# Kernel optimization log

Measured on AMD Instinct MI355X. Metric: run time of the kernel, lower is better.

Reference implementation:

```python
import jax, jax.numpy as jnp
import numpy as np

N_NODES = 100000
N_EDGES = 640000
D_IN = 128
D_HID = 128
D_OUT = 128
EPS = 1e-12  # F.normalize clamp_min eps


def _sage_conv(x, src, dst, Wl, bl, Wr):
    # mean aggregation of source features onto destination nodes
    msgs = x[src]                                              # [E, C] gather
    agg = jax.ops.segment_sum(msgs, dst, num_segments=N_NODES)  # [N, C] scatter-add
    cnt = jax.ops.segment_sum(jnp.ones((src.shape[0],), x.dtype), dst,
                              num_segments=N_NODES)
    agg = agg / jnp.maximum(cnt, 1.0)[:, None]
    out = agg @ Wl.T + bl + x @ Wr.T                           # lin_l(aggr) + lin_r(root)
    # L2 row-normalize (normalize=True)
    norm = jnp.sqrt(jnp.sum(out * out, axis=-1, keepdims=True))
    return out / jnp.maximum(norm, EPS)


def setup_inputs() -> dict:
    key = jax.random.key(0)
    ks = jax.random.split(key, 8)
    x = jax.random.normal(ks[0], (N_NODES, D_IN), dtype=jnp.float32)
    edge_index = jax.random.randint(ks[1], (2, N_EDGES), 0, N_NODES, dtype=jnp.int64)
    s1 = 1.0 / np.sqrt(D_IN)
    s2 = 1.0 / np.sqrt(D_HID)
    Wl1 = jax.random.uniform(ks[2], (D_HID, D_IN), jnp.float32, -s1, s1)
    bl1 = jax.random.uniform(ks[3], (D_HID,), jnp.float32, -s1, s1)
    Wr1 = jax.random.uniform(ks[4], (D_HID, D_IN), jnp.float32, -s1, s1)
    Wl2 = jax.random.uniform(ks[5], (D_OUT, D_HID), jnp.float32, -s2, s2)
    bl2 = jax.random.uniform(ks[6], (D_OUT,), jnp.float32, -s2, s2)
    Wr2 = jax.random.uniform(ks[7], (D_OUT, D_HID), jnp.float32, -s2, s2)
    return {"x": x, "edge_index": edge_index, "Wl1": Wl1, "bl1": bl1,
            "Wr1": Wr1, "Wl2": Wl2, "bl2": bl2, "Wr2": Wr2}


def reference(x, edge_index, Wl1, bl1, Wr1, Wl2, bl2, Wr2):
    src, dst = edge_index[0], edge_index[1]
    h = _sage_conv(x, src, dst, Wl1, bl1, Wr1)
    h = jax.nn.relu(h)  # dropout is identity in eval mode
    h = _sage_conv(h, src, dst, Wl2, bl2, Wr2)
    return h
```

## Files before the change

### kernel.cpp

```cpp
#include <hip/hip_runtime.h>
#include <hip/hip_bf16.h>
#include <stdint.h>

#define N_NODES 100000
#define N_EDGES 640000
#define MPAD    100096
#define CNT4_BLOCKS (N_EDGES / 1024)
#define CONV4_T     (N_NODES * 32)
#define CONV4_BLOCKS ((CONV4_T + 255) / 256)

typedef short  bf8_t  __attribute__((ext_vector_type(8)));
typedef float  f32x4  __attribute__((ext_vector_type(4)));

__device__ __forceinline__ unsigned f2bf(float f) {
  unsigned u = __builtin_bit_cast(unsigned, f);
  return ((u + 0x7fffu + ((u >> 16) & 1u)) >> 16) & 0xffffu;
}
__device__ __forceinline__ float bf2f(unsigned bits) {
  return __builtin_bit_cast(float, bits << 16);
}

__global__ void k_count_conv(const int* __restrict__ dst, int* __restrict__ cnt,
                             const float* __restrict__ x, unsigned* __restrict__ A1,
                             const float* __restrict__ Wl1, const float* __restrict__ Wr1,
                             unsigned short* __restrict__ Bf1,
                             const float* __restrict__ Wl2, const float* __restrict__ Wr2,
                             unsigned short* __restrict__ Bf2) {
  int bx = blockIdx.x;
  if (bx < CNT4_BLOCKS) {
    int base = bx * 1024 + threadIdx.x;
    int d0 = dst[base], d1 = dst[base + 256], d2 = dst[base + 512], d3 = dst[base + 768];
    atomicAdd(&cnt[d0], 1);
    atomicAdd(&cnt[d1], 1);
    atomicAdd(&cnt[d2], 1);
    atomicAdd(&cnt[d3], 1);
    return;
  }
  if (bx < CNT4_BLOCKS + CONV4_BLOCKS) {
    int i = (bx - CNT4_BLOCKS) * 256 + threadIdx.x;
    if (i < CONV4_T) {
      int w = i >> 5, t = i & 31;
      float4 f = ((const float4*)x)[i];
      uint2 u;
      u.x = f2bf(f.x) | (f2bf(f.y) << 16);
      u.y = f2bf(f.z) | (f2bf(f.w) << 16);
      ((uint2*)A1)[(size_t)w * 64 + 32 + t] = u;
    }
    return;
  }
  int gid = (bx - CNT4_BLOCKS - CONV4_BLOCKS) * 256 + threadIdx.x;
  if (gid >= 8192) return;
  int tid = gid & 4095;
  const float* Wl = (gid < 4096) ? Wl1 : Wl2;
  const float* Wr = (gid < 4096) ? Wr1 : Wr2;
  unsigned short* Bf = (gid < 4096) ? Bf1 : Bf2;
  int lane = tid & 63;
  int t  = (tid >> 6) & 7;
  int kc = tid >> 9;
  int c = lane & 15, q = lane >> 4;
  int col = t * 16 + c;
  for (int j = 0; j < 8; ++j) {
    int k = kc * 32 + q * 8 + j;
    float v = (k < 128) ? Wl[col * 128 + k] : Wr[col * 128 + (k - 128)];
    Bf[(size_t)tid * 8 + j] = (unsigned short)f2bf(v);
  }
}

__global__ void k_bsum(const int* __restrict__ cnt, int* __restrict__ bsum) {
  __shared__ int s[256];
  int base = blockIdx.x * 1024;
  int t = threadIdx.x;
  int v = 0;
  for (int j = 0; j < 4; ++j) {
    int i = base + j * 256 + t;
    if (i < N_NODES) v += cnt[i];
  }
  s[t] = v; __syncthreads();
  for (int o = 128; o > 0; o >>= 1) { if (t < o) s[t] += s[t + o]; __syncthreads(); }
  if (t == 0) bsum[blockIdx.x] = s[0];
}

__global__ void k_scanb(int* __restrict__ bsum, int nb) {
  __shared__ int s[128];
  int t = threadIdx.x;
  int v = (t < nb) ? bsum[t] : 0;
  s[t] = v; __syncthreads();
  for (int o = 1; o < 128; o <<= 1) {
    int add = (t >= o) ? s[t - o] : 0;
    __syncthreads();
    s[t] += add;
    __syncthreads();
  }
  if (t < nb) bsum[t] = s[t] - v;
}

__global__ void k_scanchunk(const int* __restrict__ cnt, const int* __restrict__ bsum,
                            int* __restrict__ rowptr, float* __restrict__ inv,
                            int* __restrict__ cursor) {
  __shared__ int s[1024];
  int t = threadIdx.x;
  int i = blockIdx.x * 1024 + t;
  int v = (i < N_NODES) ? cnt[i] : 0;
  s[t] = v; __syncthreads();
  for (int o = 1; o < 1024; o <<= 1) {
    int add = (t >= o) ? s[t - o] : 0;
    __syncthreads();
    s[t] += add;
    __syncthreads();
  }
  int incl = s[t];
  int bofs = bsum[blockIdx.x];
  if (i < N_NODES) {
    int start = bofs + incl - v;
    rowptr[i] = start;
    inv[i] = 1.0f / fmaxf((float)v, 1.0f);
    cursor[i] = start;
  }
  if (i == N_NODES - 1) rowptr[N_NODES] = bofs + incl;
}

__global__ void k_scatter(const int* __restrict__ src, const int* __restrict__ dst,
                          int* __restrict__ cursor, int* __restrict__ esrc) {
  int base = blockIdx.x * 1024 + threadIdx.x;
  int d0 = dst[base],       d1 = dst[base + 256];
  int d2 = dst[base + 512], d3 = dst[base + 768];
  int s0 = src[base],       s1 = src[base + 256];
  int s2 = src[base + 512], s3 = src[base + 768];
  int p0 = atomicAdd(&cursor[d0], 1);
  int p1 = atomicAdd(&cursor[d1], 1);
  int p2 = atomicAdd(&cursor[d2], 1);
  int p3 = atomicAdd(&cursor[d3], 1);
  esrc[p0] = s0; esrc[p1] = s1; esrc[p2] = s2; esrc[p3] = s3;
}

__global__ __launch_bounds__(256) void k_agg(unsigned* __restrict__ A,
    const int* __restrict__ rowptr, const int* __restrict__ esrc,
    const float* __restrict__ inv) {
  int w = (blockIdx.x * blockDim.x + threadIdx.x) >> 6;
  int lane = threadIdx.x & 63;
  if (w >= N_NODES) return;
  int b = rowptr[w], e = rowptr[w + 1];
  int deg = e - b;
  int myi = (lane < deg) ? esrc[b + lane] : 0;
  float ax = 0.f, ay = 0.f;
  int n = (deg < 64) ? deg : 64;
  for (int j0 = 0; j0 < n; j0 += 8) {
    unsigned u[8];
#pragma unroll
    for (int j = 0; j < 8; ++j) {
      int s = __shfl(myi, j0 + j);
      u[j] = A[(size_t)s * 128 + 64 + lane];
    }
#pragma unroll
    for (int j = 0; j < 8; ++j) {
      if (j0 + j < n) { ax += bf2f(u[j] & 0xffffu); ay += bf2f(u[j] >> 16); }
    }
  }
  for (int j = b + 64; j < e; ++j) {
    int s = esrc[j];
    unsigned u = A[(size_t)s * 128 + 64 + lane];
    ax += bf2f(u & 0xffffu); ay += bf2f(u >> 16);
  }
  float iv = inv[w];
  A[(size_t)w * 128 + lane] = f2bf(ax * iv) | (f2bf(ay * iv) << 16);
}

template<int LAYER>
__global__ __launch_bounds__(256) void k_gemm(const unsigned short* __restrict__ A,
    const unsigned short* __restrict__ Bf, const float* __restrict__ bias,
    void* __restrict__ outp) {
  __shared__ unsigned short Bs[32768];
  int wid = threadIdx.x >> 6;
  int lane = threadIdx.x & 63;
  int c = lane & 15, q = lane >> 4;
  int m0 = blockIdx.x * 128 + wid * 32;

  bf8_t a0[8], a1[8];
#pragma unroll
  for (int kc = 0; kc < 8; ++kc) {
    a0[kc] = *(const bf8_t*)(A + (size_t)(m0 + c) * 256 + kc * 32 + q * 8);
    a1[kc] = *(const bf8_t*)(A + (size_t)(m0 + 16 + c) * 256 + kc * 32 + q * 8);
  }
#pragma unroll
  for (int i = 0; i < 16; ++i)
    ((bf8_t*)Bs)[i * 256 + threadIdx.x] = ((const bf8_t*)Bf)[i * 256 + threadIdx.x];
  __syncthreads();

  f32x4 acc[2][8];
#pragma unroll
  for (int h = 0; h < 2; ++h)
#pragma unroll
    for (int t = 0; t < 8; ++t) acc[h][t] = (f32x4){0.f, 0.f, 0.f, 0.f};
  const bf8_t* Bv = (const bf8_t*)Bs;
#pragma unroll
  for (int kc = 0; kc < 8; ++kc) {
#pragma unroll
    for (int t = 0; t < 8; ++t) {
      bf8_t b = Bv[(kc * 8 + t) * 64 + lane];
      acc[0][t] = __builtin_amdgcn_mfma_f32_16x16x32_bf16(a0[kc], b, acc[0][t], 0, 0, 0);
      acc[1][t] = __builtin_amdgcn_mfma_f32_16x16x32_bf16(a1[kc], b, acc[1][t], 0, 0, 0);
    }
  }
  float bcol[8];
#pragma unroll
  for (int t = 0; t < 8; ++t) bcol[t] = bias[t * 16 + c];
#pragma unroll
  for (int h = 0; h < 2; ++h) {
#pragma unroll
    for (int r = 0; r < 4; ++r) {
      float ss = 0.f;
#pragma unroll
      for (int t = 0; t < 8; ++t) {
        float v = acc[h][t][r] + bcol[t];
        acc[h][t][r] = v;
        ss += v * v;
      }
#pragma unroll
      for (int m = 1; m < 16; m <<= 1) ss += __shfl_xor(ss, m, 64);
      float invn = 1.0f / fmaxf(sqrtf(ss), 1e-12f);
      int row = m0 + h * 16 + q * 4 + r;
      if (LAYER == 1) {
        unsigned* o32 = (unsigned*)outp;
#pragma unroll
        for (int t = 0; t < 8; ++t) {
          float v = fmaxf(acc[h][t][r] * invn, 0.f);
          float vp = __shfl_xor(v, 1, 64);
          if (row < N_NODES && !(c & 1))
            o32[(size_t)row * 128 + 64 + t * 8 + (c >> 1)] = f2bf(v) | (f2bf(vp) << 16);
        }
      } else {
        float* o = (float*)outp;
        if (row < N_NODES) {
#pragma unroll
          for (int t = 0; t < 8; ++t)
            o[(size_t)row * 128 + t * 16 + c] = acc[h][t][r] * invn;
        }
      }
    }
  }
}

extern "C" void kernel_launch(void* const* d_in, const int* in_sizes, int n_in,
                              void* d_out, int out_size, void* d_ws, size_t ws_size,
                              hipStream_t stream) {
  const float* x   = (const float*)d_in[0];
  const int*   ei  = (const int*)d_in[1];
  const int*   src = ei;
  const int*   dst = ei + N_EDGES;
  const float* Wl1 = (const float*)d_in[2];
  const float* bl1 = (const float*)d_in[3];
  const float* Wr1 = (const float*)d_in[4];
  const float* Wl2 = (const float*)d_in[5];
  const float* bl2 = (const float*)d_in[6];
  const float* Wr2 = (const float*)d_in[7];

  char* ws = (char*)d_ws;
  size_t off = 0;
  auto alloc = [&](size_t bytes) -> void* {
    void* p = ws + off;
    off += (bytes + 255) & ~(size_t)255;
    return p;
  };
  unsigned short* A1  = (unsigned short*)alloc((size_t)MPAD * 256 * 2);
  unsigned short* A2  = (unsigned short*)alloc((size_t)MPAD * 256 * 2);
  unsigned short* Bf1 = (unsigned short*)alloc(65536);
  unsigned short* Bf2 = (unsigned short*)alloc(65536);
  int*   esrc   = (int*)alloc((size_t)N_EDGES * 4);
  int*   rowptr = (int*)alloc((size_t)(N_NODES + 1) * 4);
  int*   cnt    = (int*)alloc((size_t)N_NODES * 4);
  int*   cursor = (int*)alloc((size_t)N_NODES * 4);
  float* inv    = (float*)alloc((size_t)N_NODES * 4);
  int*   bsum   = (int*)alloc(1024);

  hipMemsetAsync(cnt, 0, (size_t)N_NODES * 4, stream);

  const int NB = (N_NODES + 1023) / 1024;
  k_count_conv<<<CNT4_BLOCKS + CONV4_BLOCKS + 32, 256, 0, stream>>>(
                 dst, cnt, x, (unsigned*)A1, Wl1, Wr1, Bf1, Wl2, Wr2, Bf2);
  k_bsum      <<<NB, 256, 0, stream>>>(cnt, bsum);
  k_scanb     <<<1, 128, 0, stream>>>(bsum, NB);
  k_scanchunk <<<NB, 1024, 0, stream>>>(cnt, bsum, rowptr, inv, cursor);
  k_scatter   <<<CNT4_BLOCKS, 256, 0, stream>>>(src, dst, cursor, esrc);

  k_agg    <<<(N_NODES * 64 + 255) / 256, 256, 0, stream>>>((unsigned*)A1, rowptr, esrc, inv);
  k_gemm<1><<<MPAD / 128, 256, 0, stream>>>(A1, Bf1, bl1, A2);
  k_agg    <<<(N_NODES * 64 + 255) / 256, 256, 0, stream>>>((unsigned*)A2, rowptr, esrc, inv);
  k_gemm<2><<<MPAD / 128, 256, 0, stream>>>(A2, Bf2, bl2, d_out);
}
```

Measured before the change: 292.3 us.

## Record per-edge rank during counting to drop scatter atomics and cursor array

```diff
diff --git a/kernel.cpp b/kernel.cpp
--- a/kernel.cpp
+++ b/kernel.cpp
@@ -7,7 +7,8 @@
 #define MPAD    100096
 #define CNT4_BLOCKS (N_EDGES / 1024)
 #define CONV4_T     (N_NODES * 32)
-#define CONV4_BLOCKS ((CONV4_T + 255) / 256)
+#define CONV_STRIDE (CONV4_T / 4)
+#define CONV_BLOCKS (CONV_STRIDE / 256)
 
 typedef short  bf8_t  __attribute__((ext_vector_type(8)));
 typedef float  f32x4  __attribute__((ext_vector_type(4)));
@@ -21,6 +22,7 @@
 }
 
 __global__ void k_count_conv(const int* __restrict__ dst, int* __restrict__ cnt,
+                             int* __restrict__ rank,
                              const float* __restrict__ x, unsigned* __restrict__ A1,
                              const float* __restrict__ Wl1, const float* __restrict__ Wr1,
                              unsigned short* __restrict__ Bf1,
@@ -30,25 +32,34 @@
   if (bx < CNT4_BLOCKS) {
     int base = bx * 1024 + threadIdx.x;
     int d0 = dst[base], d1 = dst[base + 256], d2 = dst[base + 512], d3 = dst[base + 768];
-    atomicAdd(&cnt[d0], 1);
-    atomicAdd(&cnt[d1], 1);
-    atomicAdd(&cnt[d2], 1);
-    atomicAdd(&cnt[d3], 1);
+    int r0 = atomicAdd(&cnt[d0], 1);
+    int r1 = atomicAdd(&cnt[d1], 1);
+    int r2 = atomicAdd(&cnt[d2], 1);
+    int r3 = atomicAdd(&cnt[d3], 1);
+    rank[base]       = r0;
+    rank[base + 256] = r1;
+    rank[base + 512] = r2;
+    rank[base + 768] = r3;
     return;
   }
-  if (bx < CNT4_BLOCKS + CONV4_BLOCKS) {
-    int i = (bx - CNT4_BLOCKS) * 256 + threadIdx.x;
-    if (i < CONV4_T) {
+  if (bx < CNT4_BLOCKS + CONV_BLOCKS) {
+    int g = (bx - CNT4_BLOCKS) * 256 + threadIdx.x;
+    float4 f[4];
+#pragma unroll
+    for (int j = 0; j < 4; ++j)
+      f[j] = ((const float4*)x)[g + j * CONV_STRIDE];
+#pragma unroll
+    for (int j = 0; j < 4; ++j) {
+      int i = g + j * CONV_STRIDE;
       int w = i >> 5, t = i & 31;
-      float4 f = ((const float4*)x)[i];
       uint2 u;
-      u.x = f2bf(f.x) | (f2bf(f.y) << 16);
-      u.y = f2bf(f.z) | (f2bf(f.w) << 16);
+      u.x = f2bf(f[j].x) | (f2bf(f[j].y) << 16);
+      u.y = f2bf(f[j].z) | (f2bf(f[j].w) << 16);
       ((uint2*)A1)[(size_t)w * 64 + 32 + t] = u;
     }
     return;
   }
-  int gid = (bx - CNT4_BLOCKS - CONV4_BLOCKS) * 256 + threadIdx.x;
+  int gid = (bx - CNT4_BLOCKS - CONV_BLOCKS) * 256 + threadIdx.x;
   if (gid >= 8192) return;
   int tid = gid & 4095;
   const float* Wl = (gid < 4096) ? Wl1 : Wl2;
@@ -95,8 +106,7 @@
 }
 
 __global__ void k_scanchunk(const int* __restrict__ cnt, const int* __restrict__ bsum,
-                            int* __restrict__ rowptr, float* __restrict__ inv,
-                            int* __restrict__ cursor) {
+                            int* __restrict__ rowptr, float* __restrict__ inv) {
   __shared__ int s[1024];
   int t = threadIdx.x;
   int i = blockIdx.x * 1024 + t;
@@ -111,25 +121,26 @@
   int incl = s[t];
   int bofs = bsum[blockIdx.x];
   if (i < N_NODES) {
-    int start = bofs + incl - v;
-    rowptr[i] = start;
+    rowptr[i] = bofs + incl - v;
     inv[i] = 1.0f / fmaxf((float)v, 1.0f);
-    cursor[i] = start;
   }
   if (i == N_NODES - 1) rowptr[N_NODES] = bofs + incl;
 }
 
 __global__ void k_scatter(const int* __restrict__ src, const int* __restrict__ dst,
-                          int* __restrict__ cursor, int* __restrict__ esrc) {
+                          const int* __restrict__ rank, const int* __restrict__ rowptr,
+                          int* __restrict__ esrc) {
   int base = blockIdx.x * 1024 + threadIdx.x;
   int d0 = dst[base],       d1 = dst[base + 256];
   int d2 = dst[base + 512], d3 = dst[base + 768];
   int s0 = src[base],       s1 = src[base + 256];
   int s2 = src[base + 512], s3 = src[base + 768];
-  int p0 = atomicAdd(&cursor[d0], 1);
-  int p1 = atomicAdd(&cursor[d1], 1);
-  int p2 = atomicAdd(&cursor[d2], 1);
-  int p3 = atomicAdd(&cursor[d3], 1);
+  int r0 = rank[base],      r1 = rank[base + 256];
+  int r2 = rank[base + 512], r3 = rank[base + 768];
+  int p0 = rowptr[d0] + r0;
+  int p1 = rowptr[d1] + r1;
+  int p2 = rowptr[d2] + r2;
+  int p3 = rowptr[d3] + r3;
   esrc[p0] = s0; esrc[p1] = s1; esrc[p2] = s2; esrc[p3] = s3;
 }
 
@@ -266,21 +277,21 @@
   unsigned short* Bf1 = (unsigned short*)alloc(65536);
   unsigned short* Bf2 = (unsigned short*)alloc(65536);
   int*   esrc   = (int*)alloc((size_t)N_EDGES * 4);
+  int*   rank   = (int*)alloc((size_t)N_EDGES * 4);
   int*   rowptr = (int*)alloc((size_t)(N_NODES + 1) * 4);
   int*   cnt    = (int*)alloc((size_t)N_NODES * 4);
-  int*   cursor = (int*)alloc((size_t)N_NODES * 4);
   float* inv    = (float*)alloc((size_t)N_NODES * 4);
   int*   bsum   = (int*)alloc(1024);
 
   hipMemsetAsync(cnt, 0, (size_t)N_NODES * 4, stream);
 
   const int NB = (N_NODES + 1023) / 1024;
-  k_count_conv<<<CNT4_BLOCKS + CONV4_BLOCKS + 32, 256, 0, stream>>>(
-                 dst, cnt, x, (unsigned*)A1, Wl1, Wr1, Bf1, Wl2, Wr2, Bf2);
+  k_count_conv<<<CNT4_BLOCKS + CONV_BLOCKS + 32, 256, 0, stream>>>(
+                 dst, cnt, rank, x, (unsigned*)A1, Wl1, Wr1, Bf1, Wl2, Wr2, Bf2);
   k_bsum      <<<NB, 256, 0, stream>>>(cnt, bsum);
   k_scanb     <<<1, 128, 0, stream>>>(bsum, NB);
-  k_scanchunk <<<NB, 1024, 0, stream>>>(cnt, bsum, rowptr, inv, cursor);
-  k_scatter   <<<CNT4_BLOCKS, 256, 0, stream>>>(src, dst, cursor, esrc);
+  k_scanchunk <<<NB, 1024, 0, stream>>>(cnt, bsum, rowptr, inv);
+  k_scatter   <<<CNT4_BLOCKS, 256, 0, stream>>>(src, dst, rank, rowptr, esrc);
 
   k_agg    <<<(N_NODES * 64 + 255) / 256, 256, 0, stream>>>((unsigned*)A1, rowptr, esrc, inv);
   k_gemm<1><<<MPAD / 128, 256, 0, stream>>>(A1, Bf1, bl1, A2);
```

Result: faster. 275.3 us (-5.8%).
